# Performance work log

Hardware: AMD Instinct MI355X
Metric: run time of the kernel (lower is better)

## Reference

```python
import jax, jax.numpy as jnp
import numpy as np

B, S, D = 4, 512, 256

def setup_inputs() -> dict:
    key = jax.random.key(0)
    ks = jax.random.split(key, 32)
    def w(k, shape, s=0.05):
        return jax.random.normal(k, shape, dtype=jnp.float32) * s
    inp = {
        "img": jax.random.normal(ks[0], (B, S, D), dtype=jnp.float32),
        "audio": jax.random.normal(ks[1], (B, S, D), dtype=jnp.float32),
        "common": jax.random.normal(ks[2], (B, S, D), dtype=jnp.float32),
    }
    names = ["qv", "qa", "kv", "ka", "cc", "w5", "w6", "w7", "w8"]
    for i, n in enumerate(names):
        inp[n + "_w"] = w(ks[3 + 2 * i], (D, D))   # stored [in, out]
        inp[n + "_b"] = w(ks[4 + 2 * i], (D,))
    inp["bil_w"] = w(ks[25], (D, D, D))            # Bilinear weight [out, in1, in2]
    inp["t_o"] = jnp.ones((), dtype=jnp.float32)
    return inp


def reference(img, audio, common,
              qv_w, qv_b, qa_w, qa_b, kv_w, kv_b, ka_w, ka_b, cc_w, cc_b,
              w5_w, w5_b, w6_w, w6_b, w7_w, w7_b, w8_w, w8_b,
              bil_w, t_o):
    dim_k = qv_w.shape[1]
    norm_fact = 1.0 / jnp.sqrt(jnp.asarray(dim_k, dtype=jnp.float32))

    lin = lambda x, w, b: x @ w + b
    # NOTE: faithful to source - softmax first, THEN scaled by norm_fact.
    attn = lambda q, k: jax.nn.softmax(jnp.einsum('bsd,btd->bst', q, k), axis=-1) * norm_fact

    W_q_v = lin(img, qv_w, qv_b)
    W_q_a = lin(audio, qa_w, qa_b)
    w_k_a = lin(audio, ka_w, ka_b)
    W_k_v = lin(img, kv_w, kv_b)
    C_c = lin(common, cc_w, cc_b)

    atten_vv = attn(W_q_v, W_k_v)
    atten_vc = attn(W_q_v, C_c)
    atten_aa = attn(W_q_a, w_k_a)
    atten_ac = attn(W_q_a, C_c)

    vc_common = jnp.einsum('bst,btd->bsd', atten_vc, common)
    ac_common = jnp.einsum('bst,btd->bsd', atten_ac, common)

    common_feat_v = (1.0 + lin(vc_common, w5_w, w5_b)) * jnp.einsum('bst,btd->bsd', atten_vv, img) + lin(vc_common, w6_w, w6_b)
    common_feat_a = (1.0 + lin(ac_common, w7_w, w7_b)) * jnp.einsum('bst,btd->bsd', atten_aa, audio) + lin(ac_common, w8_w, w8_b)

    # Bilinear: out[b,s,k] = v[b,s,:] @ W[k] @ a[b,s,:]
    atten_m = jnp.einsum('bsi,kij,bsj->bsk', common_feat_v, bil_w, common_feat_a)
    j_o = jax.nn.sigmoid(atten_m)
    Z_k_o = t_o * j_o * img + (1.0 - j_o) * audio
    return (Z_k_o + img, Z_k_o + audio)
```

## Files before the change

### kernel.cpp

```cpp
#include <hip/hip_runtime.h>
#include <hip/hip_bf16.h>

typedef unsigned short ushortT;
typedef __bf16 bf16x8 __attribute__((ext_vector_type(8)));
typedef float f32x4 __attribute__((ext_vector_type(4)));
typedef ushortT ush8 __attribute__((ext_vector_type(8)));
typedef ushortT ush4 __attribute__((ext_vector_type(4)));

#define MFMA16(a, b, c) __builtin_amdgcn_mfma_f32_16x16x32_bf16((a), (b), (c), 0, 0, 0)

__device__ __forceinline__ ushortT f2b(float f) {
  __hip_bfloat16 h = __float2bfloat16(f);
  return __builtin_bit_cast(ushortT, h);
}
__device__ __forceinline__ float b2f(ushortT u) {
  __hip_bfloat16 h = __builtin_bit_cast(__hip_bfloat16, u);
  return __bfloat162float(h);
}

__device__ __forceinline__ void async16(const void* g, void* l) {
  __builtin_amdgcn_global_load_lds((const __attribute__((address_space(1))) unsigned int*)g,
                                   (__attribute__((address_space(3))) unsigned int*)l, 16, 0, 0);
}

#define ACT_E 524288
#define WD_E  65536

#define OFF_ACT16   0u
#define OFF_ACTT16  3145728u
#define OFF_W16T    6291456u
#define OFF_PROJ16  7471104u
#define OFF_P16     12713984u
#define OFF_VC16    21102592u
#define OFF_AC16    22151168u
#define OFF_PVV32   23199744u
#define OFF_PVA32   25296896u
#define OFF_PART    0u
#define OFF_BIL16   33554432u
#define OFF_CFV16   67108864u
#define OFF_CFA16   68157440u

__global__ void k_cvt_acts(const float* __restrict__ img, const float* __restrict__ aud,
                           const float* __restrict__ com, ushortT* __restrict__ dst) {
  int i4 = blockIdx.x * 256 + threadIdx.x;
#pragma unroll
  for (int q = 0; q < 4; q++) {
    int idx4 = i4 + q * 98304;
    int flat = idx4 * 4;
    const float* src;
    int off;
    if (flat < 524288)        { src = img; off = flat; }
    else if (flat < 1048576)  { src = aud; off = flat - 524288; }
    else                      { src = com; off = flat - 1048576; }
    float4 v = *(const float4*)(src + off);
    ush4 u = { f2b(v.x), f2b(v.y), f2b(v.z), f2b(v.w) };
    *(ush4*)(dst + idx4 * 4) = u;
  }
}

__global__ void k_cvt_bil(const float* __restrict__ bil, ushortT* __restrict__ dst) {
  int i4 = blockIdx.x * 256 + threadIdx.x;
#pragma unroll
  for (int q = 0; q < 8; q++) {
    int idx4 = i4 + q * 524288;
    float4 v = *(const float4*)(bil + idx4 * 4);
    ush4 u = { f2b(v.x), f2b(v.y), f2b(v.z), f2b(v.w) };
    *(ush4*)(dst + idx4 * 4) = u;
  }
}

__global__ void k_transpose(const float* __restrict__ img, const float* __restrict__ aud,
                            const float* __restrict__ com,
                            const float* w0, const float* w1, const float* w2,
                            const float* w3, const float* w4, const float* w5,
                            const float* w6, const float* w7, const float* w8,
                            ushortT* __restrict__ actT, ushortT* __restrict__ wT) {
  __shared__ ushortT tl[64][72];
  int tid = threadIdx.x;
  int bx = blockIdx.x;
  const float* src;
  ushortT* dst;
  int R, C, r0, c0;
  if (bx < 384) {
    int inst = bx >> 5, tile = bx & 31;
    int act = inst >> 2, bb = inst & 3;
    src = (act == 0 ? img : (act == 1 ? aud : com)) + bb * 131072;
    dst = actT + act * 524288 + bb * 131072;
    R = 512; C = 256;
    r0 = (tile >> 2) * 64; c0 = (tile & 3) * 64;
  } else {
    int bw = bx - 384;
    int w = bw >> 4, tile = bw & 15;
    const float* s;
    switch (w) {
      case 0: s = w0; break; case 1: s = w1; break; case 2: s = w2; break;
      case 3: s = w3; break; case 4: s = w4; break; case 5: s = w5; break;
      case 6: s = w6; break; case 7: s = w7; break; default: s = w8; break;
    }
    src = s;
    dst = wT + w * 65536;
    R = 256; C = 256;
    r0 = (tile >> 2) * 64; c0 = (tile & 3) * 64;
  }
#pragma unroll
  for (int q = 0; q < 4; q++) {
    int rr = q * 16 + (tid >> 4);
    int cs = (tid & 15) * 4;
    float4 v = *(const float4*)(src + (r0 + rr) * C + c0 + cs);
    tl[rr][cs + 0] = f2b(v.x);
    tl[rr][cs + 1] = f2b(v.y);
    tl[rr][cs + 2] = f2b(v.z);
    tl[rr][cs + 3] = f2b(v.w);
  }
  __syncthreads();
#pragma unroll
  for (int q = 0; q < 4; q++) {
    int cc = q * 16 + (tid >> 4);
    int rs = (tid & 15) * 4;
    ush4 u = { tl[rs + 0][cc], tl[rs + 1][cc], tl[rs + 2][cc], tl[rs + 3][cc] };
    *(ush4*)(dst + (c0 + cc) * R + r0 + rs) = u;
  }
}

__global__ __launch_bounds__(512) void k_linear5(
    const ushortT* __restrict__ act16, const ushortT* __restrict__ wT,
    const float* __restrict__ b0, const float* __restrict__ b1,
    const float* __restrict__ b2, const float* __restrict__ b3,
    const float* __restrict__ b4, ushortT* __restrict__ proj16) {
  __shared__ ushortT Al[4][32][8];
  __shared__ ushortT Bl[4][256][8];
  const int tid = threadIdx.x, l = tid & 63, w = tid >> 6;
  const int bx = blockIdx.x;
  const int op = bx >> 6, sblk = bx & 63;
  const int s0 = sblk * 32;
  const int xsel = (op == 4) ? 2 : (op & 1);
  const ushortT* X = act16 + xsel * ACT_E;
  const ushortT* W = wT + op * WD_E;
  const float* bias = op == 0 ? b0 : op == 1 ? b1 : op == 2 ? b2 : op == 3 ? b3 : b4;
  ushortT* out = proj16 + op * ACT_E;

  f32x4 acc[2][2] = {};
  ush8 ra, rb[2];
  int a_row = tid >> 2, a_seg = tid & 3;

  auto sload = [&](int k0) {
    if (tid < 128) ra = *(const ush8*)(X + (s0 + a_row) * 256 + k0 + a_seg * 8);
#pragma unroll
    for (int q = 0; q < 2; q++) {
      int slot = tid + q * 512;
      rb[q] = *(const ush8*)(W + (slot >> 2) * 256 + k0 + (slot & 3) * 8);
    }
  };
  auto swrite = [&]() {
    if (tid < 128) *(ush8*)(&Al[a_seg][a_row][0]) = ra;
#pragma unroll
    for (int q = 0; q < 2; q++) {
      int slot = tid + q * 512;
      *(ush8*)(&Bl[slot & 3][slot >> 2][0]) = rb[q];
    }
  };

  sload(0); swrite(); __syncthreads();
  for (int s = 0; s < 8; s++) {
    if (s < 7) sload((s + 1) * 32);
    int ks = l >> 4;
    bf16x8 a[2], bb[2];
#pragma unroll
    for (int m = 0; m < 2; m++) a[m] = *(const bf16x8*)(&Al[ks][m * 16 + (l & 15)][0]);
#pragma unroll
    for (int n = 0; n < 2; n++) bb[n] = *(const bf16x8*)(&Bl[ks][w * 32 + n * 16 + (l & 15)][0]);
#pragma unroll
    for (int m = 0; m < 2; m++)
#pragma unroll
      for (int n = 0; n < 2; n++) acc[m][n] = MFMA16(a[m], bb[n], acc[m][n]);
    if (s == 7) break;
    __syncthreads();
    swrite();
    __syncthreads();
  }
#pragma unroll
  for (int m = 0; m < 2; m++)
#pragma unroll
    for (int n = 0; n < 2; n++)
#pragma unroll
      for (int r = 0; r < 4; r++) {
        int row = s0 + m * 16 + (l >> 4) * 4 + r;
        int col = w * 32 + n * 16 + (l & 15);
        out[row * 256 + col] = f2b(acc[m][n][r] + bias[col]);
      }
}

__global__ __launch_bounds__(512) void k_attn(const ushortT* __restrict__ proj16,
                                              ushortT* __restrict__ P16) {
  __shared__ ushortT Ql[8][4][32][8];
  __shared__ ushortT Kl[4][512][8];
  __shared__ float red[32][8];
  const int tid = threadIdx.x, l = tid & 63, w = tid >> 6;
  const int bx = blockIdx.x;
  const int p = bx >> 6, b = (bx >> 4) & 3, sblk = bx & 15;
  const int s0 = sblk * 32;
  const int qsel = (p < 2) ? 0 : 1;
  const int ksel = (p == 0) ? 2 : (p == 2) ? 3 : 4;
  const ushortT* Q = proj16 + qsel * ACT_E + b * 131072;
  const ushortT* K = proj16 + ksel * ACT_E + b * 131072;
  ushortT* P = P16 + p * 1048576 + b * 262144;

#pragma unroll
  for (int q = 0; q < 2; q++) {
    int slot = tid + q * 512;
    int row = slot >> 5, seg = slot & 31;
    ush8 v = *(const ush8*)(Q + (s0 + row) * 256 + seg * 8);
    *(ush8*)(&Ql[seg >> 2][seg & 3][row][0]) = v;
  }

  f32x4 acc[2][4] = {};
  ush8 rk[4];
  auto kload = [&](int d0) {
#pragma unroll
    for (int q = 0; q < 4; q++) {
      int slot = tid + q * 512;
      rk[q] = *(const ush8*)(K + (slot >> 2) * 256 + d0 + (slot & 3) * 8);
    }
  };
  auto kwrite = [&]() {
#pragma unroll
    for (int q = 0; q < 4; q++) {
      int slot = tid + q * 512;
      *(ush8*)(&Kl[slot & 3][slot >> 2][0]) = rk[q];
    }
  };

  kload(0); kwrite(); __syncthreads();
  for (int s = 0; s < 8; s++) {
    if (s < 7) kload((s + 1) * 32);
    int ks = l >> 4;
    bf16x8 a[2], bb[4];
#pragma unroll
    for (int m = 0; m < 2; m++) a[m] = *(const bf16x8*)(&Ql[s][ks][m * 16 + (l & 15)][0]);
#pragma unroll
    for (int n = 0; n < 4; n++) bb[n] = *(const bf16x8*)(&Kl[ks][w * 64 + n * 16 + (l & 15)][0]);
#pragma unroll
    for (int m = 0; m < 2; m++)
#pragma unroll
      for (int n = 0; n < 4; n++) acc[m][n] = MFMA16(a[m], bb[n], acc[m][n]);
    if (s == 7) break;
    __syncthreads();
    kwrite();
    __syncthreads();
  }

  float gmax[2][4];
#pragma unroll
  for (int m = 0; m < 2; m++)
#pragma unroll
    for (int r = 0; r < 4; r++) {
      float v = fmaxf(fmaxf(acc[m][0][r], acc[m][1][r]), fmaxf(acc[m][2][r], acc[m][3][r]));
#pragma unroll
      for (int off = 1; off < 16; off <<= 1) v = fmaxf(v, __shfl_xor(v, off, 16));
      if ((l & 15) == 0) red[m * 16 + (l >> 4) * 4 + r][w] = v;
    }
  __syncthreads();
#pragma unroll
  for (int m = 0; m < 2; m++)
#pragma unroll
    for (int r = 0; r < 4; r++) {
      int sr = m * 16 + (l >> 4) * 4 + r;
      float g = red[sr][0];
#pragma unroll
      for (int ww = 1; ww < 8; ww++) g = fmaxf(g, red[sr][ww]);
      gmax[m][r] = g;
    }
  __syncthreads();
#pragma unroll
  for (int m = 0; m < 2; m++)
#pragma unroll
    for (int r = 0; r < 4; r++) {
      float ssum = 0.f;
#pragma unroll
      for (int n = 0; n < 4; n++) {
        float e = __expf(acc[m][n][r] - gmax[m][r]);
        acc[m][n][r] = e;
        ssum += e;
      }
#pragma unroll
      for (int off = 1; off < 16; off <<= 1) ssum += __shfl_xor(ssum, off, 16);
      if ((l & 15) == 0) red[m * 16 + (l >> 4) * 4 + r][w] = ssum;
    }
  __syncthreads();
#pragma unroll
  for (int m = 0; m < 2; m++)
#pragma unroll
    for (int r = 0; r < 4; r++) {
      int sr = m * 16 + (l >> 4) * 4 + r;
      float tot = 0.f;
#pragma unroll
      for (int ww = 0; ww < 8; ww++) tot += red[sr][ww];
      float sc = 0.0625f / tot;
#pragma unroll
      for (int n = 0; n < 4; n++)
        P[(s0 + sr) * 512 + w * 64 + n * 16 + (l & 15)] = f2b(acc[m][n][r] * sc);
    }
}

__global__ __launch_bounds__(512) void k_pv(const ushortT* __restrict__ P16,
                                            const ushortT* __restrict__ actT,
                                            float* __restrict__ pvv, float* __restrict__ pva,
                                            ushortT* __restrict__ vc16, ushortT* __restrict__ ac16) {
  __shared__ ushortT Al[4][32][8];
  __shared__ ushortT Bl[4][256][8];
  const int tid = threadIdx.x, l = tid & 63, w = tid >> 6;
  const int bx = blockIdx.x;
  const int p = bx >> 6, b = (bx >> 4) & 3, sblk = bx & 15;
  const int s0 = sblk * 32;
  const ushortT* A = P16 + p * 1048576 + b * 262144;
  const int vsel = (p == 0) ? 0 : (p == 2) ? 1 : 2;
  const ushortT* VT = actT + vsel * ACT_E + b * 131072;

  f32x4 acc[2][2] = {};
  ush8 ra, rb[2];
  int a_row = tid >> 2, a_seg = tid & 3;
  auto sload = [&](int t0) {
    if (tid < 128) ra = *(const ush8*)(A + (s0 + a_row) * 512 + t0 + a_seg * 8);
#pragma unroll
    for (int q = 0; q < 2; q++) {
      int slot = tid + q * 512;
      rb[q] = *(const ush8*)(VT + (slot >> 2) * 512 + t0 + (slot & 3) * 8);
    }
  };
  auto swrite = [&]() {
    if (tid < 128) *(ush8*)(&Al[a_seg][a_row][0]) = ra;
#pragma unroll
    for (int q = 0; q < 2; q++) {
      int slot = tid + q * 512;
      *(ush8*)(&Bl[slot & 3][slot >> 2][0]) = rb[q];
    }
  };

  sload(0); swrite(); __syncthreads();
  for (int s = 0; s < 16; s++) {
    if (s < 15) sload((s + 1) * 32);
    int ks = l >> 4;
    bf16x8 a[2], bb[2];
#pragma unroll
    for (int m = 0; m < 2; m++) a[m] = *(const bf16x8*)(&Al[ks][m * 16 + (l & 15)][0]);
#pragma unroll
    for (int n = 0; n < 2; n++) bb[n] = *(const bf16x8*)(&Bl[ks][w * 32 + n * 16 + (l & 15)][0]);
#pragma unroll
    for (int m = 0; m < 2; m++)
#pragma unroll
      for (int n = 0; n < 2; n++) acc[m][n] = MFMA16(a[m], bb[n], acc[m][n]);
    if (s == 15) break;
    __syncthreads();
    swrite();
    __syncthreads();
  }
#pragma unroll
  for (int m = 0; m < 2; m++)
#pragma unroll
    for (int n = 0; n < 2; n++)
#pragma unroll
      for (int r = 0; r < 4; r++) {
        int row = s0 + m * 16 + (l >> 4) * 4 + r;
        int col = w * 32 + n * 16 + (l & 15);
        int gi = (b * 512 + row) * 256 + col;
        float v = acc[m][n][r];
        if (p == 0) pvv[gi] = v;
        else if (p == 1) vc16[gi] = f2b(v);
        else if (p == 2) pva[gi] = v;
        else ac16[gi] = f2b(v);
      }
}

__global__ __launch_bounds__(512) void k_lin4c(
    const ushortT* __restrict__ vc16, const ushortT* __restrict__ ac16,
    const ushortT* __restrict__ wT,
    const float* __restrict__ w5b, const float* __restrict__ w6b,
    const float* __restrict__ w7b, const float* __restrict__ w8b,
    const float* __restrict__ pvv, const float* __restrict__ pva,
    ushortT* __restrict__ cfv, ushortT* __restrict__ cfa) {
  __shared__ ushortT Al[4][32][8];
  __shared__ ushortT B1[4][256][8];
  __shared__ ushortT B2[4][256][8];
  const int tid = threadIdx.x, l = tid & 63, w = tid >> 6;
  const int bx = blockIdx.x;
  const int side = bx >> 6, sblk = bx & 63;
  const int s0 = sblk * 32;
  const ushortT* A = side ? ac16 : vc16;
  const ushortT* W1 = wT + (side ? 7 : 5) * WD_E;
  const ushortT* W2 = wT + (side ? 8 : 6) * WD_E;
  const float* bb1 = side ? w7b : w5b;
  const float* bb2 = side ? w8b : w6b;
  const float* pv = side ? pva : pvv;
  ushortT* out = side ? cfa : cfv;

  f32x4 acc1[2][2] = {}, acc2[2][2] = {};
  ush8 ra, rb1[2], rb2[2];
  int a_row = tid >> 2, a_seg = tid & 3;
  auto sload = [&](int k0) {
    if (tid < 128) ra = *(const ush8*)(A + (s0 + a_row) * 256 + k0 + a_seg * 8);
#pragma unroll
    for (int q = 0; q < 2; q++) {
      int slot = tid + q * 512;
      rb1[q] = *(const ush8*)(W1 + (slot >> 2) * 256 + k0 + (slot & 3) * 8);
      rb2[q] = *(const ush8*)(W2 + (slot >> 2) * 256 + k0 + (slot & 3) * 8);
    }
  };
  auto swrite = [&]() {
    if (tid < 128) *(ush8*)(&Al[a_seg][a_row][0]) = ra;
#pragma unroll
    for (int q = 0; q < 2; q++) {
      int slot = tid + q * 512;
      *(ush8*)(&B1[slot & 3][slot >> 2][0]) = rb1[q];
      *(ush8*)(&B2[slot & 3][slot >> 2][0]) = rb2[q];
    }
  };

  sload(0); swrite(); __syncthreads();
  for (int s = 0; s < 8; s++) {
    if (s < 7) sload((s + 1) * 32);
    int ks = l >> 4;
    bf16x8 a[2], x1[2], x2[2];
#pragma unroll
    for (int m = 0; m < 2; m++) a[m] = *(const bf16x8*)(&Al[ks][m * 16 + (l & 15)][0]);
#pragma unroll
    for (int n = 0; n < 2; n++) {
      x1[n] = *(const bf16x8*)(&B1[ks][w * 32 + n * 16 + (l & 15)][0]);
      x2[n] = *(const bf16x8*)(&B2[ks][w * 32 + n * 16 + (l & 15)][0]);
    }
#pragma unroll
    for (int m = 0; m < 2; m++)
#pragma unroll
      for (int n = 0; n < 2; n++) {
        acc1[m][n] = MFMA16(a[m], x1[n], acc1[m][n]);
        acc2[m][n] = MFMA16(a[m], x2[n], acc2[m][n]);
      }
    if (s == 7) break;
    __syncthreads();
    swrite();
    __syncthreads();
  }
#pragma unroll
  for (int m = 0; m < 2; m++)
#pragma unroll
    for (int n = 0; n < 2; n++)
#pragma unroll
      for (int r = 0; r < 4; r++) {
        int row = s0 + m * 16 + (l >> 4) * 4 + r;
        int col = w * 32 + n * 16 + (l & 15);
        int gi = row * 256 + col;
        float u1 = acc1[m][n][r] + bb1[col];
        float u2 = acc2[m][n][r] + bb2[col];
        out[gi] = f2b((1.f + u1) * pv[gi] + u2);
      }
}

__global__ __launch_bounds__(512, 2) void k_bilinear5(
    const ushortT* __restrict__ cfa, const ushortT* __restrict__ cfv,
    const ushortT* __restrict__ W, float* __restrict__ part) {
  __shared__ char arena[155648];
  const int tid = threadIdx.x, l = tid & 63, w = tid >> 6;
  const int d = blockIdx.x;
  const int L = (d & 7) * 32 + (d >> 3);
  const int ic = L >> 4;
  const int mb = (L >> 1) & 7;
  const int nb = L & 1;
  const int r0 = mb * 256;
  const int ko0 = nb * 128;
  const int wr = w >> 1, wc = w & 1;

  ushortT* cfvl = (ushortT*)(arena + 147456);
  {
    int row = tid >> 1, seg = tid & 1;
    *(ush8*)(cfvl + row * 16 + seg * 8) =
        *(const ush8*)(cfv + (r0 + row) * 256 + ic * 16 + seg * 8);
  }
  __syncthreads();

  const char* gA[4];
  const char* gB[2];
#pragma unroll
  for (int s = 0; s < 4; s++) {
    int p = (tid + s * 512) * 16;
    int lg = p ^ (((p >> 7) & 7) << 4);
    gA[s] = (const char*)cfa + (size_t)(r0 + (lg >> 7)) * 512 + (lg & 127);
  }
#pragma unroll
  for (int s = 0; s < 2; s++) {
    int p = (tid + s * 512) * 16;
    int lg = p ^ (((p >> 7) & 7) << 4);
    gB[s] = (const char*)W + (size_t)(ko0 + (lg >> 7)) * 131072 + (size_t)ic * 8192 + (lg & 127);
  }

  auto stage = [&](int t) {
    char* Ab = arena + (t % 3) * 32768;
    char* Bb = arena + 98304 + (t % 3) * 16384;
    int ja = (t & 3) << 7;
    int jb = t << 7;
#pragma unroll
    for (int s = 0; s < 4; s++) async16(gA[s] + ja, Ab + (tid + s * 512) * 16);
#pragma unroll
    for (int s = 0; s < 2; s++) async16(gB[s] + jb, Bb + (tid + s * 512) * 16);
  };

  int aoff[2][4], boff[2][4];
#pragma unroll
  for (int m = 0; m < 4; m++) {
    int row = wr * 64 + m * 16 + (l & 15);
    int b0 = row * 128 + (l >> 4) * 16;
    int msk = (row & 7) << 4;
    aoff[0][m] = b0 ^ msk;
    aoff[1][m] = (b0 + 64) ^ msk;
  }
#pragma unroll
  for (int n = 0; n < 4; n++) {
    int row = wc * 64 + n * 16 + (l & 15);
    int b0 = row * 128 + (l >> 4) * 16;
    int msk = (row & 7) << 4;
    boff[0][n] = b0 ^ msk;
    boff[1][n] = (b0 + 64) ^ msk;
  }

  f32x4 macc[4][4] = {};
  f32x4 acci[4][4] = {};

  stage(0);
  stage(1);

  for (int t = 0; t < 64; t++) {
    if (t < 62) asm volatile("s_waitcnt vmcnt(6)" ::: "memory");
    else        asm volatile("s_waitcnt vmcnt(0)" ::: "memory");
    __builtin_amdgcn_s_barrier();

    char* Ab = arena + (t % 3) * 32768;
    char* Bb = arena + 98304 + (t % 3) * 16384;

    bf16x8 a0[4], b0v[4];
#pragma unroll
    for (int m = 0; m < 4; m++) a0[m] = *(const bf16x8*)(Ab + aoff[0][m]);
#pragma unroll
    for (int n = 0; n < 4; n++) b0v[n] = *(const bf16x8*)(Bb + boff[0][n]);
    __builtin_amdgcn_s_setprio(1);
#pragma unroll
    for (int m = 0; m < 4; m++)
#pragma unroll
      for (int n = 0; n < 4; n++) acci[m][n] = MFMA16(a0[m], b0v[n], acci[m][n]);
    __builtin_amdgcn_s_setprio(0);

    if (t + 2 < 64) stage(t + 2);

    bf16x8 a1[4], b1v[4];
#pragma unroll
    for (int m = 0; m < 4; m++) a1[m] = *(const bf16x8*)(Ab + aoff[1][m]);
#pragma unroll
    for (int n = 0; n < 4; n++) b1v[n] = *(const bf16x8*)(Bb + boff[1][n]);
    __builtin_amdgcn_s_setprio(1);
#pragma unroll
    for (int m = 0; m < 4; m++)
#pragma unroll
      for (int n = 0; n < 4; n++) acci[m][n] = MFMA16(a1[m], b1v[n], acci[m][n]);
    __builtin_amdgcn_s_setprio(0);

    if ((t & 3) == 3) {
      int il = t >> 2;
#pragma unroll
      for (int m = 0; m < 4; m++) {
        int rbase = wr * 64 + m * 16 + ((l >> 4) << 2);
        float c0 = b2f(cfvl[(rbase + 0) * 16 + il]);
        float c1 = b2f(cfvl[(rbase + 1) * 16 + il]);
        float c2 = b2f(cfvl[(rbase + 2) * 16 + il]);
        float c3 = b2f(cfvl[(rbase + 3) * 16 + il]);
#pragma unroll
        for (int n = 0; n < 4; n++) {
          macc[m][n][0] += c0 * acci[m][n][0];
          macc[m][n][1] += c1 * acci[m][n][1];
          macc[m][n][2] += c2 * acci[m][n][2];
          macc[m][n][3] += c3 * acci[m][n][3];
          acci[m][n] = (f32x4){0.f, 0.f, 0.f, 0.f};
        }
      }
    }
  }

  float* dst = part + (size_t)ic * 524288 + (size_t)r0 * 256 + ko0;
#pragma unroll
  for (int m = 0; m < 4; m++)
#pragma unroll
    for (int n = 0; n < 4; n++)
#pragma unroll
      for (int r = 0; r < 4; r++)
        dst[(wr * 64 + m * 16 + ((l >> 4) << 2) + r) * 256 + wc * 64 + n * 16 + (l & 15)] =
            macc[m][n][r];
}

__global__ void k_final2(const float* __restrict__ part, const float* __restrict__ img,
                         const float* __restrict__ aud, const float* __restrict__ t_o,
                         float* __restrict__ out0, float* __restrict__ out1) {
  int i = blockIdx.x * 256 + threadIdx.x;
  float t = t_o[0];
  float4 m = {0.f, 0.f, 0.f, 0.f};
#pragma unroll
  for (int ic = 0; ic < 16; ic++) {
    float4 p = ((const float4*)(part + ic * 524288))[i];
    m.x += p.x; m.y += p.y; m.z += p.z; m.w += p.w;
  }
  float4 a = ((const float4*)img)[i];
  float4 u = ((const float4*)aud)[i];
  float4 o0, o1;
  {
    float j = 1.f / (1.f + __expf(-m.x)); float Z = t * j * a.x + (1.f - j) * u.x;
    o0.x = Z + a.x; o1.x = Z + u.x;
  }
  {
    float j = 1.f / (1.f + __expf(-m.y)); float Z = t * j * a.y + (1.f - j) * u.y;
    o0.y = Z + a.y; o1.y = Z + u.y;
  }
  {
    float j = 1.f / (1.f + __expf(-m.z)); float Z = t * j * a.z + (1.f - j) * u.z;
    o0.z = Z + a.z; o1.z = Z + u.z;
  }
  {
    float j = 1.f / (1.f + __expf(-m.w)); float Z = t * j * a.w + (1.f - j) * u.w;
    o0.w = Z + a.w; o1.w = Z + u.w;
  }
  ((float4*)out0)[i] = o0;
  ((float4*)out1)[i] = o1;
}

extern "C" void kernel_launch(void* const* d_in, const int* in_sizes, int n_in,
                              void* d_out, int out_size, void* d_ws, size_t ws_size,
                              hipStream_t stream) {
  const float* img   = (const float*)d_in[0];
  const float* aud   = (const float*)d_in[1];
  const float* com   = (const float*)d_in[2];
  const float* qv_w  = (const float*)d_in[3];
  const float* qv_b  = (const float*)d_in[4];
  const float* qa_w  = (const float*)d_in[5];
  const float* qa_b  = (const float*)d_in[6];
  const float* kv_w  = (const float*)d_in[7];
  const float* kv_b  = (const float*)d_in[8];
  const float* ka_w  = (const float*)d_in[9];
  const float* ka_b  = (const float*)d_in[10];
  const float* cc_w  = (const float*)d_in[11];
  const float* cc_b  = (const float*)d_in[12];
  const float* w5_w  = (const float*)d_in[13];
  const float* w5_b  = (const float*)d_in[14];
  const float* w6_w  = (const float*)d_in[15];
  const float* w6_b  = (const float*)d_in[16];
  const float* w7_w  = (const float*)d_in[17];
  const float* w7_b  = (const float*)d_in[18];
  const float* w8_w  = (const float*)d_in[19];
  const float* w8_b  = (const float*)d_in[20];
  const float* bil_w = (const float*)d_in[21];
  const float* t_o   = (const float*)d_in[22];
  float* out = (float*)d_out;

  char* ws = (char*)d_ws;
  ushortT* act16  = (ushortT*)(ws + OFF_ACT16);
  ushortT* actT16 = (ushortT*)(ws + OFF_ACTT16);
  ushortT* w16t   = (ushortT*)(ws + OFF_W16T);
  ushortT* proj16 = (ushortT*)(ws + OFF_PROJ16);
  ushortT* P16    = (ushortT*)(ws + OFF_P16);
  ushortT* vc16   = (ushortT*)(ws + OFF_VC16);
  ushortT* ac16   = (ushortT*)(ws + OFF_AC16);
  float*   pvv32  = (float*)(ws + OFF_PVV32);
  float*   pva32  = (float*)(ws + OFF_PVA32);
  float*   part   = (float*)(ws + OFF_PART);
  ushortT* bil16  = (ushortT*)(ws + OFF_BIL16);
  ushortT* cfv16  = (ushortT*)(ws + OFF_CFV16);
  ushortT* cfa16  = (ushortT*)(ws + OFF_CFA16);

  k_cvt_acts<<<384, 256, 0, stream>>>(img, aud, com, act16);
  k_cvt_bil<<<2048, 256, 0, stream>>>(bil_w, bil16);
  k_transpose<<<528, 256, 0, stream>>>(img, aud, com, qv_w, qa_w, kv_w, ka_w, cc_w,
                                       w5_w, w6_w, w7_w, w8_w, actT16, w16t);
  k_linear5<<<320, 512, 0, stream>>>(act16, w16t, qv_b, qa_b, kv_b, ka_b, cc_b, proj16);
  k_attn<<<256, 512, 0, stream>>>(proj16, P16);
  k_pv<<<256, 512, 0, stream>>>(P16, actT16, pvv32, pva32, vc16, ac16);
  k_lin4c<<<128, 512, 0, stream>>>(vc16, ac16, w16t, w5_b, w6_b, w7_b, w8_b,
                                   pvv32, pva32, cfv16, cfa16);
  k_bilinear5<<<256, 512, 0, stream>>>(cfa16, cfv16, bil16, part);
  k_final2<<<512, 256, 0, stream>>>(part, img, aud, t_o, out, out + 524288);
}
```

Baseline: 150.8 us.

## Fold cfv scaling into A operand and keep cfa tiles in registers

```diff
diff --git a/kernel.cpp b/kernel.cpp
--- a/kernel.cpp
+++ b/kernel.cpp
@@ -21,6 +21,22 @@
 __device__ __forceinline__ void async16(const void* g, void* l) {
   __builtin_amdgcn_global_load_lds((const __attribute__((address_space(1))) unsigned int*)g,
                                    (__attribute__((address_space(3))) unsigned int*)l, 16, 0, 0);
+}
+
+__device__ __forceinline__ bf16x8 scale8(bf16x8 a, float s) {
+  union { bf16x8 v; unsigned int u[4]; } in, out;
+  in.v = a;
+#pragma unroll
+  for (int p = 0; p < 4; p++) {
+    float lo = __builtin_bit_cast(float, in.u[p] << 16);
+    float hi = __builtin_bit_cast(float, in.u[p] & 0xffff0000u);
+    lo *= s;
+    hi *= s;
+    unsigned int r;
+    asm("v_cvt_pk_bf16_f32 %0, %1, %2" : "=v"(r) : "v"(lo), "v"(hi));
+    out.u[p] = r;
+  }
+  return out.v;
 }
 
 #define ACT_E 524288
@@ -454,10 +470,10 @@
       }
 }
 
-__global__ __launch_bounds__(512, 2) void k_bilinear5(
+__global__ __launch_bounds__(512, 2) void k_bilinear6(
     const ushortT* __restrict__ cfa, const ushortT* __restrict__ cfv,
     const ushortT* __restrict__ W, float* __restrict__ part) {
-  __shared__ char arena[155648];
+  __shared__ char arena[66560];
   const int tid = threadIdx.x, l = tid & 63, w = tid >> 6;
   const int d = blockIdx.x;
   const int L = (d & 7) * 32 + (d >> 3);
@@ -468,49 +484,26 @@
   const int ko0 = nb * 128;
   const int wr = w >> 1, wc = w & 1;
 
-  ushortT* cfvl = (ushortT*)(arena + 147456);
+  float* cfvl = (float*)(arena + 49152);
   {
-    int row = tid >> 1, seg = tid & 1;
-    *(ush8*)(cfvl + row * 16 + seg * 8) =
-        *(const ush8*)(cfv + (r0 + row) * 256 + ic * 16 + seg * 8);
+    int row = tid >> 1, half = tid & 1;
+    ush8 v = *(const ush8*)(cfv + (r0 + row) * 256 + ic * 16 + half * 8);
+    float* dp = cfvl + row * 17 + half * 8;
+#pragma unroll
+    for (int q = 0; q < 8; q++) dp[q] = b2f(v[q]);
   }
   __syncthreads();
 
-  const char* gA[4];
   const char* gB[2];
-#pragma unroll
-  for (int s = 0; s < 4; s++) {
-    int p = (tid + s * 512) * 16;
-    int lg = p ^ (((p >> 7) & 7) << 4);
-    gA[s] = (const char*)cfa + (size_t)(r0 + (lg >> 7)) * 512 + (lg & 127);
-  }
+  int bdst[2];
 #pragma unroll
   for (int s = 0; s < 2; s++) {
     int p = (tid + s * 512) * 16;
     int lg = p ^ (((p >> 7) & 7) << 4);
     gB[s] = (const char*)W + (size_t)(ko0 + (lg >> 7)) * 131072 + (size_t)ic * 8192 + (lg & 127);
-  }
-
-  auto stage = [&](int t) {
-    char* Ab = arena + (t % 3) * 32768;
-    char* Bb = arena + 98304 + (t % 3) * 16384;
-    int ja = (t & 3) << 7;
-    int jb = t << 7;
-#pragma unroll
-    for (int s = 0; s < 4; s++) async16(gA[s] + ja, Ab + (tid + s * 512) * 16);
-#pragma unroll
-    for (int s = 0; s < 2; s++) async16(gB[s] + jb, Bb + (tid + s * 512) * 16);
-  };
-
-  int aoff[2][4], boff[2][4];
-#pragma unroll
-  for (int m = 0; m < 4; m++) {
-    int row = wr * 64 + m * 16 + (l & 15);
-    int b0 = row * 128 + (l >> 4) * 16;
-    int msk = (row & 7) << 4;
-    aoff[0][m] = b0 ^ msk;
-    aoff[1][m] = (b0 + 64) ^ msk;
-  }
+    bdst[s] = p;
+  }
+  int boff[2][4];
 #pragma unroll
   for (int n = 0; n < 4; n++) {
     int row = wc * 64 + n * 16 + (l & 15);
@@ -520,63 +513,81 @@
     boff[1][n] = (b0 + 64) ^ msk;
   }
 
+  const ushortT* gA = cfa + (size_t)(r0 + wr * 64 + (l & 15)) * 256 + (l >> 4) * 8;
+  const float* cfvp = cfvl + (wr * 64 + (l & 15)) * 17;
+
+  auto stageT = [&](int t) {
+    char* Bb = arena + (t % 3) * 16384;
+    int jb = ((t >> 4) << 7) + ((t & 15) << 9);
+    async16(gB[0] + jb, Bb + bdst[0]);
+    async16(gB[1] + jb, Bb + bdst[1]);
+  };
+
+  bf16x8 ab[8], an[8];
+#pragma unroll
+  for (int kc = 0; kc < 2; kc++)
+#pragma unroll
+    for (int mf = 0; mf < 4; mf++)
+      ab[kc * 4 + mf] = *(const bf16x8*)(gA + mf * 4096 + kc * 32);
+
+  stageT(0);
+  stageT(1);
+
   f32x4 macc[4][4] = {};
-  f32x4 acci[4][4] = {};
-
-  stage(0);
-  stage(1);
-
-  for (int t = 0; t < 64; t++) {
-    if (t < 62) asm volatile("s_waitcnt vmcnt(6)" ::: "memory");
-    else        asm volatile("s_waitcnt vmcnt(0)" ::: "memory");
-    __builtin_amdgcn_s_barrier();
-
-    char* Ab = arena + (t % 3) * 32768;
-    char* Bb = arena + 98304 + (t % 3) * 16384;
-
-    bf16x8 a0[4], b0v[4];
-#pragma unroll
-    for (int m = 0; m < 4; m++) a0[m] = *(const bf16x8*)(Ab + aoff[0][m]);
-#pragma unroll
-    for (int n = 0; n < 4; n++) b0v[n] = *(const bf16x8*)(Bb + boff[0][n]);
-    __builtin_amdgcn_s_setprio(1);
-#pragma unroll
-    for (int m = 0; m < 4; m++)
-#pragma unroll
-      for (int n = 0; n < 4; n++) acci[m][n] = MFMA16(a0[m], b0v[n], acci[m][n]);
-    __builtin_amdgcn_s_setprio(0);
-
-    if (t + 2 < 64) stage(t + 2);
-
-    bf16x8 a1[4], b1v[4];
-#pragma unroll
-    for (int m = 0; m < 4; m++) a1[m] = *(const bf16x8*)(Ab + aoff[1][m]);
-#pragma unroll
-    for (int n = 0; n < 4; n++) b1v[n] = *(const bf16x8*)(Bb + boff[1][n]);
-    __builtin_amdgcn_s_setprio(1);
-#pragma unroll
-    for (int m = 0; m < 4; m++)
-#pragma unroll
-      for (int n = 0; n < 4; n++) acci[m][n] = MFMA16(a1[m], b1v[n], acci[m][n]);
-    __builtin_amdgcn_s_setprio(0);
-
-    if ((t & 3) == 3) {
-      int il = t >> 2;
-#pragma unroll
-      for (int m = 0; m < 4; m++) {
-        int rbase = wr * 64 + m * 16 + ((l >> 4) << 2);
-        float c0 = b2f(cfvl[(rbase + 0) * 16 + il]);
-        float c1 = b2f(cfvl[(rbase + 1) * 16 + il]);
-        float c2 = b2f(cfvl[(rbase + 2) * 16 + il]);
-        float c3 = b2f(cfvl[(rbase + 3) * 16 + il]);
-#pragma unroll
-        for (int n = 0; n < 4; n++) {
-          macc[m][n][0] += c0 * acci[m][n][0];
-          macc[m][n][1] += c1 * acci[m][n][1];
-          macc[m][n][2] += c2 * acci[m][n][2];
-          macc[m][n][3] += c3 * acci[m][n][3];
-          acci[m][n] = (f32x4){0.f, 0.f, 0.f, 0.f};
+
+  for (int js = 0; js < 4; js++) {
+    if (js > 0) {
+#pragma unroll
+      for (int q = 0; q < 8; q++) ab[q] = an[q];
+    }
+#pragma unroll 4
+    for (int i = 0; i < 16; i++) {
+      const int t = js * 16 + i;
+      if (js == 3 && i == 15)      asm volatile("s_waitcnt vmcnt(0)" ::: "memory");
+      else if (i == 15)            asm volatile("s_waitcnt vmcnt(10)" ::: "memory");
+      else                         asm volatile("s_waitcnt vmcnt(2)" ::: "memory");
+      __builtin_amdgcn_s_barrier();
+
+      char* Bb = arena + (t % 3) * 16384;
+      float sc[4];
+#pragma unroll
+      for (int mf = 0; mf < 4; mf++) sc[mf] = cfvp[mf * 272 + i];
+
+      {
+        bf16x8 bf[4];
+#pragma unroll
+        for (int n = 0; n < 4; n++) bf[n] = *(const bf16x8*)(Bb + boff[0][n]);
+        __builtin_amdgcn_s_setprio(1);
+#pragma unroll
+        for (int mf = 0; mf < 4; mf++) {
+          bf16x8 as = scale8(ab[mf], sc[mf]);
+#pragma unroll
+          for (int n = 0; n < 4; n++) macc[mf][n] = MFMA16(as, bf[n], macc[mf][n]);
         }
+        __builtin_amdgcn_s_setprio(0);
+      }
+
+      if (t + 2 < 64) stageT(t + 2);
+      if (i == 14 && js < 3) {
+#pragma unroll
+        for (int kc = 0; kc < 2; kc++)
+#pragma unroll
+          for (int mf = 0; mf < 4; mf++)
+            an[kc * 4 + mf] = *(const bf16x8*)(gA + mf * 4096 + kc * 32 + (js + 1) * 64);
+      }
+
+      {
+        bf16x8 bf[4];
+#pragma unroll
+        for (int n = 0; n < 4; n++) bf[n] = *(const bf16x8*)(Bb + boff[1][n]);
+        __builtin_amdgcn_s_setprio(1);
+#pragma unroll
+        for (int mf = 0; mf < 4; mf++) {
+          bf16x8 as = scale8(ab[4 + mf], sc[mf]);
+#pragma unroll
+          for (int n = 0; n < 4; n++) macc[mf][n] = MFMA16(as, bf[n], macc[mf][n]);
+        }
+        __builtin_amdgcn_s_setprio(0);
       }
     }
   }
@@ -678,6 +689,6 @@
   k_pv<<<256, 512, 0, stream>>>(P16, actT16, pvv32, pva32, vc16, ac16);
   k_lin4c<<<128, 512, 0, stream>>>(vc16, ac16, w16t, w5_b, w6_b, w7_b, w8_b,
                                    pvv32, pva32, cfv16, cfa16);
-  k_bilinear5<<<256, 512, 0, stream>>>(cfa16, cfv16, bil16, part);
+  k_bilinear6<<<256, 512, 0, stream>>>(cfa16, cfv16, bil16, part);
   k_final2<<<512, 256, 0, stream>>>(part, img, aud, t_o, out, out + 524288);
 }
```

Result: slower. 168.8 us (+11.9%).

## Fuse bilinear weight bf16 conversion and cfv scaling into bilinear kernel

Applied to the files above, without the earlier changes.

```diff
diff --git a/kernel.cpp b/kernel.cpp
--- a/kernel.cpp
+++ b/kernel.cpp
@@ -18,9 +18,30 @@
   return __bfloat162float(h);
 }
 
-__device__ __forceinline__ void async16(const void* g, void* l) {
-  __builtin_amdgcn_global_load_lds((const __attribute__((address_space(1))) unsigned int*)g,
-                                   (__attribute__((address_space(3))) unsigned int*)l, 16, 0, 0);
+__device__ __forceinline__ bf16x8 scale8(bf16x8 a, float s) {
+  union { bf16x8 v; unsigned int u[4]; } in, out;
+  in.v = a;
+#pragma unroll
+  for (int p = 0; p < 4; p++) {
+    float lo = __builtin_bit_cast(float, in.u[p] << 16);
+    float hi = __builtin_bit_cast(float, in.u[p] & 0xffff0000u);
+    lo *= s;
+    hi *= s;
+    unsigned int r;
+    asm("v_cvt_pk_bf16_f32 %0, %1, %2" : "=v"(r) : "v"(lo), "v"(hi));
+    out.u[p] = r;
+  }
+  return out.v;
+}
+
+__device__ __forceinline__ void packB16(const f32x4 lo, const f32x4 hi, void* dst) {
+  unsigned int o0, o1, o2, o3;
+  asm("v_cvt_pk_bf16_f32 %0, %1, %2" : "=v"(o0) : "v"(lo[0]), "v"(lo[1]));
+  asm("v_cvt_pk_bf16_f32 %0, %1, %2" : "=v"(o1) : "v"(lo[2]), "v"(lo[3]));
+  asm("v_cvt_pk_bf16_f32 %0, %1, %2" : "=v"(o2) : "v"(hi[0]), "v"(hi[1]));
+  asm("v_cvt_pk_bf16_f32 %0, %1, %2" : "=v"(o3) : "v"(hi[2]), "v"(hi[3]));
+  uint4 u; u.x = o0; u.y = o1; u.z = o2; u.w = o3;
+  *(uint4*)dst = u;
 }
 
 #define ACT_E 524288
@@ -36,7 +57,6 @@
 #define OFF_PVV32   23199744u
 #define OFF_PVA32   25296896u
 #define OFF_PART    0u
-#define OFF_BIL16   33554432u
 #define OFF_CFV16   67108864u
 #define OFF_CFA16   68157440u
 
@@ -53,17 +73,6 @@
     else if (flat < 1048576)  { src = aud; off = flat - 524288; }
     else                      { src = com; off = flat - 1048576; }
     float4 v = *(const float4*)(src + off);
-    ush4 u = { f2b(v.x), f2b(v.y), f2b(v.z), f2b(v.w) };
-    *(ush4*)(dst + idx4 * 4) = u;
-  }
-}
-
-__global__ void k_cvt_bil(const float* __restrict__ bil, ushortT* __restrict__ dst) {
-  int i4 = blockIdx.x * 256 + threadIdx.x;
-#pragma unroll
-  for (int q = 0; q < 8; q++) {
-    int idx4 = i4 + q * 524288;
-    float4 v = *(const float4*)(bil + idx4 * 4);
     ush4 u = { f2b(v.x), f2b(v.y), f2b(v.z), f2b(v.w) };
     *(ush4*)(dst + idx4 * 4) = u;
   }
@@ -454,55 +463,42 @@
       }
 }
 
-__global__ __launch_bounds__(512, 2) void k_bilinear5(
+__global__ __launch_bounds__(512, 2) void k_bilinear7(
     const ushortT* __restrict__ cfa, const ushortT* __restrict__ cfv,
-    const ushortT* __restrict__ W, float* __restrict__ part) {
-  __shared__ char arena[155648];
+    const float* __restrict__ Wf, float* __restrict__ part) {
+  __shared__ char arena[140288];
   const int tid = threadIdx.x, l = tid & 63, w = tid >> 6;
   const int d = blockIdx.x;
   const int L = (d & 7) * 32 + (d >> 3);
-  const int ic = L >> 4;
-  const int mb = (L >> 1) & 7;
-  const int nb = L & 1;
+  const int ic = L >> 3;
+  const int mb = L & 7;
   const int r0 = mb * 256;
-  const int ko0 = nb * 128;
+  const int icb = ic * 8;
   const int wr = w >> 1, wc = w & 1;
 
-  ushortT* cfvl = (ushortT*)(arena + 147456);
-  {
-    int row = tid >> 1, seg = tid & 1;
-    *(ush8*)(cfvl + row * 16 + seg * 8) =
-        *(const ush8*)(cfv + (r0 + row) * 256 + ic * 16 + seg * 8);
-  }
-  __syncthreads();
-
-  const char* gA[4];
-  const char* gB[2];
+  float* cfvl = (float*)(arena + 131072);
+  if (tid < 256) {
+    ush8 v = *(const ush8*)(cfv + (r0 + tid) * 256 + icb);
+    float* dp = cfvl + tid * 9;
+#pragma unroll
+    for (int q = 0; q < 8; q++) dp[q] = b2f(v[q]);
+  }
+
+  int pS[4], rowA[4];
+  const char* gAsrc[4];
+  const char* gBsrc[4];
 #pragma unroll
   for (int s = 0; s < 4; s++) {
     int p = (tid + s * 512) * 16;
     int lg = p ^ (((p >> 7) & 7) << 4);
-    gA[s] = (const char*)cfa + (size_t)(r0 + (lg >> 7)) * 512 + (lg & 127);
-  }
-#pragma unroll
-  for (int s = 0; s < 2; s++) {
-    int p = (tid + s * 512) * 16;
-    int lg = p ^ (((p >> 7) & 7) << 4);
-    gB[s] = (const char*)W + (size_t)(ko0 + (lg >> 7)) * 131072 + (size_t)ic * 8192 + (lg & 127);
-  }
-
-  auto stage = [&](int t) {
-    char* Ab = arena + (t % 3) * 32768;
-    char* Bb = arena + 98304 + (t % 3) * 16384;
-    int ja = (t & 3) << 7;
-    int jb = t << 7;
-#pragma unroll
-    for (int s = 0; s < 4; s++) async16(gA[s] + ja, Ab + (tid + s * 512) * 16);
-#pragma unroll
-    for (int s = 0; s < 2; s++) async16(gB[s] + jb, Bb + (tid + s * 512) * 16);
-  };
-
-  int aoff[2][4], boff[2][4];
+    int row = lg >> 7, colb = lg & 127;
+    pS[s] = p;
+    rowA[s] = row;
+    gAsrc[s] = (const char*)cfa + (size_t)(r0 + row) * 512 + colb;
+    gBsrc[s] = (const char*)Wf + ((size_t)row * 65536 + (size_t)icb * 256 + (colb >> 1)) * 4;
+  }
+
+  int aoff[2][4], boff[2][8];
 #pragma unroll
   for (int m = 0; m < 4; m++) {
     int row = wr * 64 + m * 16 + (l & 15);
@@ -512,83 +508,100 @@
     aoff[1][m] = (b0 + 64) ^ msk;
   }
 #pragma unroll
-  for (int n = 0; n < 4; n++) {
-    int row = wc * 64 + n * 16 + (l & 15);
+  for (int n = 0; n < 8; n++) {
+    int row = wc * 128 + n * 16 + (l & 15);
     int b0 = row * 128 + (l >> 4) * 16;
     int msk = (row & 7) << 4;
     boff[0][n] = b0 ^ msk;
     boff[1][n] = (b0 + 64) ^ msk;
   }
 
-  f32x4 macc[4][4] = {};
-  f32x4 acci[4][4] = {};
-
-  stage(0);
-  stage(1);
-
-  for (int t = 0; t < 64; t++) {
-    if (t < 62) asm volatile("s_waitcnt vmcnt(6)" ::: "memory");
-    else        asm volatile("s_waitcnt vmcnt(0)" ::: "memory");
-    __builtin_amdgcn_s_barrier();
-
-    char* Ab = arena + (t % 3) * 32768;
-    char* Bb = arena + 98304 + (t % 3) * 16384;
-
-    bf16x8 a0[4], b0v[4];
+  ush8 arg[4];
+  f32x4 brg[8];
+
+  auto loadA = [&](int t) {
+    int ja = (t & 3) << 7;
+#pragma unroll
+    for (int s = 0; s < 4; s++) arg[s] = *(const ush8*)(gAsrc[s] + ja);
+  };
+  auto loadB = [&](int t) {
+    int off = ((t >> 2) << 10) + ((t & 3) << 8);
+#pragma unroll
+    for (int s = 0; s < 4; s++) {
+      brg[2 * s]     = *(const f32x4*)(gBsrc[s] + off);
+      brg[2 * s + 1] = *(const f32x4*)(gBsrc[s] + off + 16);
+    }
+  };
+  auto writeA = [&](int t, char* Ab) {
+    int i = t >> 2;
+#pragma unroll
+    for (int s = 0; s < 4; s++) {
+      float sc = cfvl[rowA[s] * 9 + i];
+      bf16x8 as = scale8(__builtin_bit_cast(bf16x8, arg[s]), sc);
+      *(bf16x8*)(Ab + pS[s]) = as;
+    }
+  };
+  auto writeB = [&](char* Bb) {
+#pragma unroll
+    for (int s = 0; s < 4; s++) packB16(brg[2 * s], brg[2 * s + 1], Bb + pS[s]);
+  };
+
+  f32x4 macc[4][8] = {};
+
+  loadA(0); loadB(0);
+  __syncthreads();
+  writeA(0, arena);
+  writeB(arena + 65536);
+  __syncthreads();
+
+#pragma unroll 2
+  for (int t = 0; t < 32; t++) {
+    char* Ab = arena + ((t & 1) << 15);
+    char* Bb = arena + 65536 + ((t & 1) << 15);
+    char* An = arena + (((t + 1) & 1) << 15);
+    char* Bn = arena + 65536 + (((t + 1) & 1) << 15);
+
+    bf16x8 a0[4], b0v[8];
 #pragma unroll
     for (int m = 0; m < 4; m++) a0[m] = *(const bf16x8*)(Ab + aoff[0][m]);
 #pragma unroll
-    for (int n = 0; n < 4; n++) b0v[n] = *(const bf16x8*)(Bb + boff[0][n]);
+    for (int n = 0; n < 8; n++) b0v[n] = *(const bf16x8*)(Bb + boff[0][n]);
+
+    if (t < 31) { loadA(t + 1); loadB(t + 1); }
+
     __builtin_amdgcn_s_setprio(1);
 #pragma unroll
     for (int m = 0; m < 4; m++)
 #pragma unroll
-      for (int n = 0; n < 4; n++) acci[m][n] = MFMA16(a0[m], b0v[n], acci[m][n]);
+      for (int n = 0; n < 8; n++) macc[m][n] = MFMA16(a0[m], b0v[n], macc[m][n]);
     __builtin_amdgcn_s_setprio(0);
 
-    if (t + 2 < 64) stage(t + 2);
-
-    bf16x8 a1[4], b1v[4];
+    if (t < 31) { writeA(t + 1, An); writeB(Bn); }
+
+    bf16x8 a1[4], b1v[8];
 #pragma unroll
     for (int m = 0; m < 4; m++) a1[m] = *(const bf16x8*)(Ab + aoff[1][m]);
 #pragma unroll
-    for (int n = 0; n < 4; n++) b1v[n] = *(const bf16x8*)(Bb + boff[1][n]);
+    for (int n = 0; n < 8; n++) b1v[n] = *(const bf16x8*)(Bb + boff[1][n]);
+
     __builtin_amdgcn_s_setprio(1);
 #pragma unroll
     for (int m = 0; m < 4; m++)
 #pragma unroll
-      for (int n = 0; n < 4; n++) acci[m][n] = MFMA16(a1[m], b1v[n], acci[m][n]);
+      for (int n = 0; n < 8; n++) macc[m][n] = MFMA16(a1[m], b1v[n], macc[m][n]);
     __builtin_amdgcn_s_setprio(0);
 
-    if ((t & 3) == 3) {
-      int il = t >> 2;
-#pragma unroll
-      for (int m = 0; m < 4; m++) {
-        int rbase = wr * 64 + m * 16 + ((l >> 4) << 2);
-        float c0 = b2f(cfvl[(rbase + 0) * 16 + il]);
-        float c1 = b2f(cfvl[(rbase + 1) * 16 + il]);
-        float c2 = b2f(cfvl[(rbase + 2) * 16 + il]);
-        float c3 = b2f(cfvl[(rbase + 3) * 16 + il]);
-#pragma unroll
-        for (int n = 0; n < 4; n++) {
-          macc[m][n][0] += c0 * acci[m][n][0];
-          macc[m][n][1] += c1 * acci[m][n][1];
-          macc[m][n][2] += c2 * acci[m][n][2];
-          macc[m][n][3] += c3 * acci[m][n][3];
-          acci[m][n] = (f32x4){0.f, 0.f, 0.f, 0.f};
-        }
-      }
-    }
-  }
-
-  float* dst = part + (size_t)ic * 524288 + (size_t)r0 * 256 + ko0;
+    __syncthreads();
+  }
+
+  float* dst = part + (size_t)ic * 524288 + (size_t)r0 * 256;
 #pragma unroll
   for (int m = 0; m < 4; m++)
 #pragma unroll
-    for (int n = 0; n < 4; n++)
+    for (int n = 0; n < 8; n++)
 #pragma unroll
       for (int r = 0; r < 4; r++)
-        dst[(wr * 64 + m * 16 + ((l >> 4) << 2) + r) * 256 + wc * 64 + n * 16 + (l & 15)] =
+        dst[(wr * 64 + m * 16 + ((l >> 4) << 2) + r) * 256 + wc * 128 + n * 16 + (l & 15)] =
             macc[m][n][r];
 }
 
@@ -599,8 +612,8 @@
   float t = t_o[0];
   float4 m = {0.f, 0.f, 0.f, 0.f};
 #pragma unroll
-  for (int ic = 0; ic < 16; ic++) {
-    float4 p = ((const float4*)(part + ic * 524288))[i];
+  for (int ic = 0; ic < 32; ic++) {
+    float4 p = ((const float4*)(part + (size_t)ic * 524288))[i];
     m.x += p.x; m.y += p.y; m.z += p.z; m.w += p.w;
   }
   float4 a = ((const float4*)img)[i];
@@ -665,12 +678,10 @@
   float*   pvv32  = (float*)(ws + OFF_PVV32);
   float*   pva32  = (float*)(ws + OFF_PVA32);
   float*   part   = (float*)(ws + OFF_PART);
-  ushortT* bil16  = (ushortT*)(ws + OFF_BIL16);
   ushortT* cfv16  = (ushortT*)(ws + OFF_CFV16);
   ushortT* cfa16  = (ushortT*)(ws + OFF_CFA16);
 
   k_cvt_acts<<<384, 256, 0, stream>>>(img, aud, com, act16);
-  k_cvt_bil<<<2048, 256, 0, stream>>>(bil_w, bil16);
   k_transpose<<<528, 256, 0, stream>>>(img, aud, com, qv_w, qa_w, kv_w, ka_w, cc_w,
                                        w5_w, w6_w, w7_w, w8_w, actT16, w16t);
   k_linear5<<<320, 512, 0, stream>>>(act16, w16t, qv_b, qa_b, kv_b, ka_b, cc_b, proj16);
@@ -678,6 +689,6 @@
   k_pv<<<256, 512, 0, stream>>>(P16, actT16, pvv32, pva32, vc16, ac16);
   k_lin4c<<<128, 512, 0, stream>>>(vc16, ac16, w16t, w5_b, w6_b, w7_b, w8_b,
                                    pvv32, pva32, cfv16, cfa16);
-  k_bilinear5<<<256, 512, 0, stream>>>(cfa16, cfv16, bil16, part);
+  k_bilinear7<<<256, 512, 0, stream>>>(cfa16, cfv16, bil_w, part);
   k_final2<<<512, 256, 0, stream>>>(part, img, aud, t_o, out, out + 524288);
 }
```

Result: slower. 442.4 us (+193.3%).
